# Kernel optimization log

Measured on AMD Instinct MI355X. Metric: run time of the kernel, lower is better.

Reference implementation:

```python
import jax, jax.numpy as jnp
import numpy as np
import math

B, T, EMB, HD = 4, 2048, 2048, 128
HALF = HD // 2


def setup_inputs() -> dict:
    key = jax.random.key(0)
    ks = jax.random.split(key, 4)
    x = jax.random.normal(ks[0], (B, T, EMB), dtype=jnp.float32)
    s = 1.0 / math.sqrt(EMB)
    Wq = jax.random.normal(ks[1], (EMB, HD), dtype=jnp.float32) * s
    Wk = jax.random.normal(ks[2], (EMB, HD), dtype=jnp.float32) * s
    Wv = jax.random.normal(ks[3], (EMB, HD), dtype=jnp.float32) * s
    # Standard RoPE rotation table: theta_i = 10000^(-2i/HD), angle = pos * theta
    inv_freq = 1.0 / (10000.0 ** (np.arange(0, HALF, dtype=np.float32) / HALF))
    angles = np.arange(T, dtype=np.float32)[:, None] * inv_freq[None, :]  # [T, HALF]
    rot_cos = jnp.asarray(np.cos(angles), dtype=jnp.float32)
    rot_sin = jnp.asarray(np.sin(angles), dtype=jnp.float32)
    # Additive causal mask: 0 on/below diagonal, -1e9 above
    NEG = -1e9
    mask = jnp.where(jnp.tril(jnp.ones((T, T), dtype=bool)), 0.0, NEG).astype(jnp.float32)
    return {"x": x, "Wq": Wq, "Wk": Wk, "Wv": Wv,
            "rot_cos": rot_cos, "rot_sin": rot_sin, "mask": mask}


def _apply_rope(q, rot_cos, rot_sin):
    # q: [B, T, HD]; view last dim as HALF complex pairs and rotate
    qp = q.reshape(q.shape[0], q.shape[1], HALF, 2)
    re, im = qp[..., 0], qp[..., 1]
    out_re = re * rot_cos - im * rot_sin  # broadcast [T,HALF] over batch
    out_im = re * rot_sin + im * rot_cos
    return jnp.stack([out_re, out_im], axis=-1).reshape(q.shape)


def reference(x, Wq, Wk, Wv, rot_cos, rot_sin, mask):
    Q = x @ Wq  # [B, T, HD]
    K = x @ Wk
    V = x @ Wv
    Q = _apply_rope(Q, rot_cos, rot_sin)
    K = _apply_rope(K, rot_cos, rot_sin)
    scores = jnp.einsum('bqd,bkd->bqk', Q, K) / math.sqrt(HD)
    probs = jax.nn.softmax(scores + mask, axis=-1)  # dropout is identity in eval
    return jnp.einsum('bqk,bkd->bqd', probs, V)
```

## Files before the change

### kernel.cpp

```cpp
#include <hip/hip_runtime.h>
#include <cstddef>
#include <cstdint>

#define T_SEQ 2048
#define EMB_D 2048
#define HD_D  128

typedef __attribute__((ext_vector_type(8))) short short8;
typedef __attribute__((ext_vector_type(4))) float f32x4;
typedef __attribute__((ext_vector_type(4))) unsigned short ushort4v;
typedef __attribute__((ext_vector_type(8))) unsigned short ushort8v;

union frag_u { short8 s8; unsigned u[4]; };

static __device__ __forceinline__ unsigned short f2bf_rne(float f) {
    union { float f; unsigned u; } v; v.f = f;
    unsigned r = v.u + 0x7fffu + ((v.u >> 16) & 1u);
    return (unsigned short)(r >> 16);
}
static __device__ __forceinline__ unsigned short f2bf_fast(float f) {
    union { float f; unsigned u; } v; v.f = f;
    return (unsigned short)((v.u + 0x8000u) >> 16);
}
static __device__ __forceinline__ float bf2f(unsigned short h) {
    union { unsigned u; float f; } v; v.u = ((unsigned)h) << 16;
    return v.f;
}
static __device__ __forceinline__ unsigned pk2(float a, float b) {
    union { float f; unsigned u; } x, y; x.f = a; y.f = b;
    return __builtin_amdgcn_perm(y.u + 0x8000u, x.u + 0x8000u, 0x07060302);
}
static __device__ __forceinline__ void dma16(const void* g, void* l) {
    __builtin_amdgcn_global_load_lds(
        (const __attribute__((address_space(1))) unsigned int*)g,
        (__attribute__((address_space(3))) unsigned int*)l, 16, 0, 0);
}
#define EXP2F(x) __builtin_amdgcn_exp2f(x)

__global__ __launch_bounds__(256) void prep_weights(
    const float* __restrict__ Wq, const float* __restrict__ Wk,
    const float* __restrict__ Wv, unsigned short* __restrict__ Wt)
{
    __shared__ __attribute__((aligned(16))) unsigned short tw[64 * 132];
    const int w = blockIdx.y;
    const int k0 = blockIdx.x * 64;
    const float* W = (w == 0) ? Wq : (w == 1) ? Wk : Wv;
    const int tid = threadIdx.x;
#pragma unroll
    for (int p = 0; p < 8; p++) {
        const int f = p * 256 + tid;
        const int row = f >> 5, c4 = f & 31;
        const float4 v = *(const float4*)&W[(size_t)(k0 + row) * HD_D + c4 * 4];
        ushort4v h = { f2bf_rne(v.x), f2bf_rne(v.y), f2bf_rne(v.z), f2bf_rne(v.w) };
        *(ushort4v*)&tw[row * 132 + c4 * 4] = h;
    }
    __syncthreads();
    const int kk = (tid & 7) * 8;
#pragma unroll
    for (int p = 0; p < 4; p++) {
        const int n = p * 32 + (tid >> 3);
        ushort8v o;
#pragma unroll
        for (int jj = 0; jj < 8; jj++) o[jj] = tw[(kk + jj) * 132 + n];
        *(ushort8v*)&Wt[(size_t)w * (HD_D * EMB_D) + (size_t)n * EMB_D + k0 + kk] = o;
    }
}

__global__ __launch_bounds__(256, 2) void qkv_fused(
    const float* __restrict__ x, const unsigned short* __restrict__ Wt,
    const float* __restrict__ rcos, const float* __restrict__ rsin,
    unsigned short* __restrict__ Qb, unsigned short* __restrict__ Kb,
    unsigned short* __restrict__ Vt)
{
    __shared__ __attribute__((aligned(16))) float xs[3][64 * 64];
    __shared__ __attribute__((aligned(16))) unsigned short wsb[2][96 * 64];
    const int L = blockIdx.x;
    const int xcd = L & 7, s = L >> 3;
    const int ng = s & 3;
    const int m0 = (xcd * 16 + (s >> 2)) * 64;
    const int tid = threadIdx.x;
    const int lane = tid & 63, wave = tid >> 6;
    const int wm = wave >> 1, wn = wave & 1;
    const int l15 = lane & 15, lq = lane >> 4;

    const float* xSrc[4]; int xOff[4];
#pragma unroll
    for (int p = 0; p < 4; p++) {
        const int g = p * 256 + tid;
        const int row = g >> 4, c = g & 15;
        xSrc[p] = x + (size_t)(m0 + row) * EMB_D + (c ^ (row & 15)) * 4;
        xOff[p] = (p * 256 + wave * 64) * 4;
    }
    const unsigned short* wSrc[3]; int wOff[3];
#pragma unroll
    for (int p = 0; p < 3; p++) {
        const int g = p * 256 + tid;
        const int row = g >> 3, c = g & 7;
        wSrc[p] = Wt + (size_t)(ng * 96 + row) * EMB_D + (c ^ (row & 7)) * 8;
        wOff[p] = (p * 256 + wave * 64) * 8;
    }

    int offA[2][2][2];
#pragma unroll
    for (int i = 0; i < 2; i++)
#pragma unroll
        for (int ks = 0; ks < 2; ks++) {
            const int row = wm * 32 + i * 16 + l15;
            const int ga = ks * 8 + lq * 2;
            offA[i][ks][0] = row * 64 + ((ga)     ^ (row & 15)) * 4;
            offA[i][ks][1] = row * 64 + ((ga + 1) ^ (row & 15)) * 4;
        }
    int offB[3][2];
#pragma unroll
    for (int j = 0; j < 3; j++)
#pragma unroll
        for (int ks = 0; ks < 2; ks++) {
            const int row = wn * 48 + j * 16 + l15;
            const int gb = ks * 4 + lq;
            offB[j][ks] = row * 64 + (gb ^ (row & 7)) * 8;
        }

    f32x4 acc[2][3];
#pragma unroll
    for (int i = 0; i < 2; i++)
#pragma unroll
        for (int j = 0; j < 3; j++) acc[i][j] = (f32x4){0.f, 0.f, 0.f, 0.f};

#pragma unroll
    for (int p = 0; p < 4; p++) dma16(xSrc[p], &xs[0][xOff[p]]);
#pragma unroll
    for (int p = 0; p < 3; p++) dma16(wSrc[p], &wsb[0][wOff[p]]);
#pragma unroll
    for (int p = 0; p < 4; p++) dma16(xSrc[p] + 64, &xs[1][xOff[p]]);

#define QKV_COMPUTE(XB, WB)                                                    \
    do {                                                                       \
        frag_u A[2][2];                                                        \
        _Pragma("unroll")                                                      \
        for (int i = 0; i < 2; i++)                                            \
            _Pragma("unroll")                                                  \
            for (int ks = 0; ks < 2; ks++) {                                   \
                const f32x4 f0 = *(const f32x4*)&xs[XB][offA[i][ks][0]];       \
                const f32x4 f1 = *(const f32x4*)&xs[XB][offA[i][ks][1]];       \
                A[i][ks].u[0] = pk2(f0.x, f0.y);                               \
                A[i][ks].u[1] = pk2(f0.z, f0.w);                               \
                A[i][ks].u[2] = pk2(f1.x, f1.y);                               \
                A[i][ks].u[3] = pk2(f1.z, f1.w);                               \
            }                                                                  \
        _Pragma("unroll")                                                      \
        for (int ks = 0; ks < 2; ks++)                                         \
            _Pragma("unroll")                                                  \
            for (int j = 0; j < 3; j++) {                                      \
                const short8 B = *(const short8*)&wsb[WB][offB[j][ks]];        \
                _Pragma("unroll")                                              \
                for (int i = 0; i < 2; i++)                                    \
                    acc[i][j] = __builtin_amdgcn_mfma_f32_16x16x32_bf16(       \
                        A[i][ks].s8, B, acc[i][j], 0, 0, 0);                   \
            }                                                                  \
    } while (0)

    for (int k0 = 0; k0 < EMB_D - 64; k0 += 64) {
        const int it = k0 >> 6;
        asm volatile("s_waitcnt vmcnt(4)\n\ts_barrier" ::: "memory");
#pragma unroll
        for (int p = 0; p < 3; p++)
            dma16(wSrc[p] + k0 + 64, &wsb[(it + 1) & 1][wOff[p]]);
        if (k0 + 128 < EMB_D) {
#pragma unroll
            for (int p = 0; p < 4; p++)
                dma16(xSrc[p] + k0 + 128, &xs[(it + 2) % 3][xOff[p]]);
        }
        QKV_COMPUTE(it % 3, it & 1);
    }
    asm volatile("s_waitcnt vmcnt(0)\n\ts_barrier" ::: "memory");
    QKV_COMPUTE(31 % 3, 31 & 1);
#undef QKV_COMPUTE

    const float qscale = 0.08838834764831845f * 1.4426950408889634f;
#pragma unroll
    for (int i = 0; i < 2; i++) {
#pragma unroll
        for (int r = 0; r < 4; r++) {
            const int row = m0 + wm * 32 + i * 16 + lq * 4 + r;
            const int t = row & (T_SEQ - 1);
            const int bb = row >> 11;
#pragma unroll
            for (int j = 0; j < 3; j++) {
                const int col = ng * 96 + wn * 48 + j * 16 + l15;
                const int mat = col >> 7, mcol = col & 127;
                const float v = acc[i][j][r];
                if (mat == 2) {
                    Vt[((size_t)bb * HD_D + mcol) * T_SEQ + t] = f2bf_rne(v);
                } else {
                    const int ip = mcol >> 1;
                    const float c = rcos[t * 64 + ip];
                    const float s2 = rsin[t * 64 + ip];
                    const float pv = __shfl_xor(v, 1);
                    float rv = (mcol & 1) ? (pv * s2 + v * c) : (v * c - pv * s2);
                    if (mat == 0) {
                        rv *= qscale;
                        Qb[(size_t)row * HD_D + mcol] = f2bf_rne(rv);
                    } else {
                        Kb[(size_t)row * HD_D + mcol] = f2bf_rne(rv);
                    }
                }
            }
        }
    }
}

__global__ __launch_bounds__(256, 2) void attn(
    const unsigned short* __restrict__ Qb, const unsigned short* __restrict__ Kb,
    const unsigned short* __restrict__ Vt, float* __restrict__ O0,
    unsigned short* __restrict__ O1, float* __restrict__ Lp)
{
    __shared__ __attribute__((aligned(16))) unsigned short O_s[4][16 * 128];
    __shared__ __attribute__((aligned(16))) unsigned short P_s[4][2][16 * 40];
    __shared__ float l_s[4][16];

    const int tid = threadIdx.x;
    const int lane = tid & 63, wave = tid >> 6;
    const int l15 = lane & 15, lq = lane >> 4;
    const int kf = lq * 8;

    const int L = blockIdx.x;
    const int g = L & 1;
    const int b = (L >> 1) & 3;
    const int q0 = (127 - (L >> 3)) * 16;
    const int kend = q0 + 16;
    const float M2 = 16.0f;

    const unsigned short* Qp = Qb + (size_t)(b * T_SEQ + q0) * HD_D;
    short8 aQ[4];
#pragma unroll
    for (int d = 0; d < 4; d++)
        aQ[d] = *(const short8*)&Qp[l15 * HD_D + d * 32 + kf];

    f32x4 acc[8];
#pragma unroll
    for (int d = 0; d < 8; d++) acc[d] = (f32x4){0.f, 0.f, 0.f, 0.f};
    float l_r[4] = {0.f, 0.f, 0.f, 0.f};

    const unsigned short* Kbase = Kb + (size_t)b * T_SEQ * HD_D;
    const unsigned short* Vbase = Vt + (size_t)b * HD_D * T_SEQ;
    unsigned short* PwA = &P_s[wave][0][0];
    unsigned short* PwB = &P_s[wave][1][0];

    for (int c = 2 * wave + g; c * 32 < kend; c += 16) {
        const int kA = c * 32;
        const int kB = (c + 8) * 32;
        const bool hB = kB < kend;

        const unsigned short* KpA = Kbase + (size_t)kA * HD_D;
        const unsigned short* KpB = Kbase + (size_t)kB * HD_D;
        short8 KA[8], KB_[8];
#pragma unroll
        for (int d = 0; d < 4; d++)
#pragma unroll
            for (int n = 0; n < 2; n++)
                KA[d * 2 + n] = *(const short8*)&KpA[(size_t)(n * 16 + l15) * HD_D + d * 32 + kf];
        if (hB) {
#pragma unroll
            for (int d = 0; d < 4; d++)
#pragma unroll
                for (int n = 0; n < 2; n++)
                    KB_[d * 2 + n] = *(const short8*)&KpB[(size_t)(n * 16 + l15) * HD_D + d * 32 + kf];
        }

        f32x4 sA0 = (f32x4){0.f, 0.f, 0.f, 0.f}, sA1 = sA0, sB0 = sA0, sB1 = sA0;
#pragma unroll
        for (int d = 0; d < 4; d++) {
            sA0 = __builtin_amdgcn_mfma_f32_16x16x32_bf16(aQ[d], KA[d * 2 + 0], sA0, 0, 0, 0);
            sA1 = __builtin_amdgcn_mfma_f32_16x16x32_bf16(aQ[d], KA[d * 2 + 1], sA1, 0, 0, 0);
        }
        if (hB) {
#pragma unroll
            for (int d = 0; d < 4; d++) {
                sB0 = __builtin_amdgcn_mfma_f32_16x16x32_bf16(aQ[d], KB_[d * 2 + 0], sB0, 0, 0, 0);
                sB1 = __builtin_amdgcn_mfma_f32_16x16x32_bf16(aQ[d], KB_[d * 2 + 1], sB1, 0, 0, 0);
            }
        }

        short8 VA[8];
#pragma unroll
        for (int d = 0; d < 8; d++)
            VA[d] = *(const short8*)&Vbase[(size_t)(d * 16 + l15) * T_SEQ + kA + kf];

#pragma unroll
        for (int r = 0; r < 4; r++) {
            const int q = q0 + lq * 4 + r;
            const float p0 = ((kA + l15)      <= q) ? EXP2F(sA0[r] - M2) : 0.f;
            const float p1 = ((kA + 16 + l15) <= q) ? EXP2F(sA1[r] - M2) : 0.f;
            l_r[r] += p0 + p1;
            const int prow = (lq * 4 + r) * 40;
            PwA[prow + l15]      = f2bf_fast(p0);
            PwA[prow + 16 + l15] = f2bf_fast(p1);
        }
        const short8 pA = *(const short8*)&PwA[l15 * 40 + kf];
#pragma unroll
        for (int d = 0; d < 8; d++)
            acc[d] = __builtin_amdgcn_mfma_f32_16x16x32_bf16(pA, VA[d], acc[d], 0, 0, 0);

        if (hB) {
            short8 VB[8];
#pragma unroll
            for (int d = 0; d < 8; d++)
                VB[d] = *(const short8*)&Vbase[(size_t)(d * 16 + l15) * T_SEQ + kB + kf];
#pragma unroll
            for (int r = 0; r < 4; r++) {
                const int q = q0 + lq * 4 + r;
                const float p0 = ((kB + l15)      <= q) ? EXP2F(sB0[r] - M2) : 0.f;
                const float p1 = ((kB + 16 + l15) <= q) ? EXP2F(sB1[r] - M2) : 0.f;
                l_r[r] += p0 + p1;
                const int prow = (lq * 4 + r) * 40;
                PwB[prow + l15]      = f2bf_fast(p0);
                PwB[prow + 16 + l15] = f2bf_fast(p1);
            }
            const short8 pB = *(const short8*)&PwB[l15 * 40 + kf];
#pragma unroll
            for (int d = 0; d < 8; d++)
                acc[d] = __builtin_amdgcn_mfma_f32_16x16x32_bf16(pB, VB[d], acc[d], 0, 0, 0);
        }
    }

#pragma unroll
    for (int r = 0; r < 4; r++) {
        float lr = l_r[r];
        lr += __shfl_xor(lr, 1);
        lr += __shfl_xor(lr, 2);
        lr += __shfl_xor(lr, 4);
        lr += __shfl_xor(lr, 8);
        if (l15 == 0) l_s[wave][lq * 4 + r] = lr;
#pragma unroll
        for (int d = 0; d < 8; d++)
            O_s[wave][(lq * 4 + r) * 128 + d * 16 + l15] = f2bf_fast(acc[d][r]);
    }
    __syncthreads();

    const int row = tid >> 4;
    const int dc = (tid & 15) * 8;
    const float lt = l_s[0][row] + l_s[1][row] + l_s[2][row] + l_s[3][row];
    float o[8];
#pragma unroll
    for (int k = 0; k < 8; k++) o[k] = 0.f;
#pragma unroll
    for (int w2 = 0; w2 < 4; w2++) {
        const ushort8v pv = *(const ushort8v*)&O_s[w2][row * 128 + dc];
#pragma unroll
        for (int k = 0; k < 8; k++) o[k] += bf2f(pv[k]);
    }
    const size_t grow = (size_t)(b * T_SEQ + q0 + row);
    if (g == 0) {
        float* op = O0 + grow * HD_D + dc;
#pragma unroll
        for (int k = 0; k < 8; k++) op[k] = o[k];
    } else {
        ushort8v h;
#pragma unroll
        for (int k = 0; k < 8; k++) h[k] = f2bf_fast(o[k]);
        *(ushort8v*)&O1[grow * HD_D + dc] = h;
    }
    if ((tid & 15) == 0) Lp[g * 8192 + grow] = lt;
}

__global__ __launch_bounds__(256) void attn_merge(
    float* __restrict__ out, const unsigned short* __restrict__ O1,
    const float* __restrict__ Lp)
{
    const int idx = blockIdx.x * 256 + threadIdx.x;
    const int row = idx >> 5;
    f32x4 a = ((f32x4*)out)[idx];
    const ushort4v h = ((const ushort4v*)O1)[idx];
    f32x4 bv = { bf2f(h.x), bf2f(h.y), bf2f(h.z), bf2f(h.w) };
    const float inv = 1.0f / (Lp[row] + Lp[8192 + row]);
    ((f32x4*)out)[idx] = (a + bv) * inv;
}

extern "C" void kernel_launch(void* const* d_in, const int* in_sizes, int n_in,
                              void* d_out, int out_size, void* d_ws, size_t ws_size,
                              hipStream_t stream)
{
    (void)in_sizes; (void)n_in; (void)out_size; (void)ws_size;
    const float* x  = (const float*)d_in[0];
    const float* Wq = (const float*)d_in[1];
    const float* Wk = (const float*)d_in[2];
    const float* Wv = (const float*)d_in[3];
    const float* rc = (const float*)d_in[4];
    const float* rs = (const float*)d_in[5];
    float* out = (float*)d_out;

    char* ws = (char*)d_ws;
    unsigned short* Wt = (unsigned short*)(ws);
    unsigned short* Qb = (unsigned short*)(ws + 1572864);
    unsigned short* Kb = (unsigned short*)(ws + 3670016);
    unsigned short* Vt = (unsigned short*)(ws + 5767168);
    unsigned short* O1 = (unsigned short*)(ws + 7864320);
    float*          Lp = (float*)(ws + 9961472);

    prep_weights<<<dim3(32, 3), 256, 0, stream>>>(Wq, Wk, Wv, Wt);
    qkv_fused   <<<dim3(512),   256, 0, stream>>>(x, Wt, rc, rs, Qb, Kb, Vt);
    attn        <<<dim3(1024),  256, 0, stream>>>(Qb, Kb, Vt, out, O1, Lp);
    attn_merge  <<<dim3(1024),  256, 0, stream>>>(out, O1, Lp);
}
```

Baseline: 188.4 us.

## Stage QKV GEMM tiles through registers with bf16 conversion before LDS

The QKV projection GEMM no longer uses direct global-to-LDS DMA of fp32 x tiles with per-iteration conversion. It now loads x and weight tiles into registers two steps ahead, converts x to bf16 once, and writes swizzled bf16 tiles into double-buffered LDS. Each wave then reads ready-made bf16 fragments and raises its scheduling priority around the MFMA block. This halves the LDS footprint for x, removes repeated packing in the inner loop, and may allow higher occupancy. In exchange it uses more registers for the in-flight data and adds explicit LDS store and wait steps.

```diff
diff --git a/kernel.cpp b/kernel.cpp
--- a/kernel.cpp
+++ b/kernel.cpp
@@ -10,8 +10,7 @@
 typedef __attribute__((ext_vector_type(4))) float f32x4;
 typedef __attribute__((ext_vector_type(4))) unsigned short ushort4v;
 typedef __attribute__((ext_vector_type(8))) unsigned short ushort8v;
-
-union frag_u { short8 s8; unsigned u[4]; };
+typedef __attribute__((ext_vector_type(2))) unsigned int uint2v;
 
 static __device__ __forceinline__ unsigned short f2bf_rne(float f) {
     union { float f; unsigned u; } v; v.f = f;
@@ -29,11 +28,6 @@
 static __device__ __forceinline__ unsigned pk2(float a, float b) {
     union { float f; unsigned u; } x, y; x.f = a; y.f = b;
     return __builtin_amdgcn_perm(y.u + 0x8000u, x.u + 0x8000u, 0x07060302);
-}
-static __device__ __forceinline__ void dma16(const void* g, void* l) {
-    __builtin_amdgcn_global_load_lds(
-        (const __attribute__((address_space(1))) unsigned int*)g,
-        (__attribute__((address_space(3))) unsigned int*)l, 16, 0, 0);
 }
 #define EXP2F(x) __builtin_amdgcn_exp2f(x)
 
@@ -72,8 +66,8 @@
     unsigned short* __restrict__ Qb, unsigned short* __restrict__ Kb,
     unsigned short* __restrict__ Vt)
 {
-    __shared__ __attribute__((aligned(16))) float xs[3][64 * 64];
-    __shared__ __attribute__((aligned(16))) unsigned short wsb[2][96 * 64];
+    __shared__ __attribute__((aligned(16))) unsigned short xsm[2][64 * 64];
+    __shared__ __attribute__((aligned(16))) unsigned short wsm[2][96 * 64];
     const int L = blockIdx.x;
     const int xcd = L & 7, s = L >> 3;
     const int ng = s & 3;
@@ -83,41 +77,28 @@
     const int wm = wave >> 1, wn = wave & 1;
     const int l15 = lane & 15, lq = lane >> 4;
 
-    const float* xSrc[4]; int xOff[4];
-#pragma unroll
-    for (int p = 0; p < 4; p++) {
-        const int g = p * 256 + tid;
-        const int row = g >> 4, c = g & 15;
-        xSrc[p] = x + (size_t)(m0 + row) * EMB_D + (c ^ (row & 15)) * 4;
-        xOff[p] = (p * 256 + wave * 64) * 4;
-    }
-    const unsigned short* wSrc[3]; int wOff[3];
-#pragma unroll
-    for (int p = 0; p < 3; p++) {
-        const int g = p * 256 + tid;
-        const int row = g >> 3, c = g & 7;
-        wSrc[p] = Wt + (size_t)(ng * 96 + row) * EMB_D + (c ^ (row & 7)) * 8;
-        wOff[p] = (p * 256 + wave * 64) * 8;
-    }
-
-    int offA[2][2][2];
+    const int xrow = tid >> 4, xc = tid & 15;
+    const float* xsrc = x + (size_t)(m0 + xrow) * EMB_D + xc * 4;
+    const int wrow = tid >> 3, wc = tid & 7;
+    const unsigned short* wsrc = Wt + (size_t)(ng * 96 + wrow) * EMB_D + wc * 8;
+
+    const int xw  = xrow * 128 + (((xc >> 1) ^ (xrow & 7)) << 4) + (xc & 1) * 8;
+    const int wwo = wrow * 128 + ((wc ^ (wrow & 7)) << 4);
+
+    int ra[2][2], rb[3][2];
 #pragma unroll
     for (int i = 0; i < 2; i++)
 #pragma unroll
         for (int ks = 0; ks < 2; ks++) {
             const int row = wm * 32 + i * 16 + l15;
-            const int ga = ks * 8 + lq * 2;
-            offA[i][ks][0] = row * 64 + ((ga)     ^ (row & 15)) * 4;
-            offA[i][ks][1] = row * 64 + ((ga + 1) ^ (row & 15)) * 4;
-        }
-    int offB[3][2];
-#pragma unroll
-    for (int j = 0; j < 3; j++)
+            ra[i][ks] = row * 128 + (((ks * 4 + lq) ^ (row & 7)) << 4);
+        }
+#pragma unroll
+    for (int jj = 0; jj < 3; jj++)
 #pragma unroll
         for (int ks = 0; ks < 2; ks++) {
-            const int row = wn * 48 + j * 16 + l15;
-            const int gb = ks * 4 + lq;
-            offB[j][ks] = row * 64 + (gb ^ (row & 7)) * 8;
+            const int row = wn * 48 + jj * 16 + l15;
+            rb[jj][ks] = row * 128 + (((ks * 4 + lq) ^ (row & 7)) << 4);
         }
 
     f32x4 acc[2][3];
@@ -126,55 +107,80 @@
 #pragma unroll
         for (int j = 0; j < 3; j++) acc[i][j] = (f32x4){0.f, 0.f, 0.f, 0.f};
 
-#pragma unroll
-    for (int p = 0; p < 4; p++) dma16(xSrc[p], &xs[0][xOff[p]]);
-#pragma unroll
-    for (int p = 0; p < 3; p++) dma16(wSrc[p], &wsb[0][wOff[p]]);
-#pragma unroll
-    for (int p = 0; p < 4; p++) dma16(xSrc[p] + 64, &xs[1][xOff[p]]);
-
-#define QKV_COMPUTE(XB, WB)                                                    \
-    do {                                                                       \
-        frag_u A[2][2];                                                        \
-        _Pragma("unroll")                                                      \
-        for (int i = 0; i < 2; i++)                                            \
-            _Pragma("unroll")                                                  \
-            for (int ks = 0; ks < 2; ks++) {                                   \
-                const f32x4 f0 = *(const f32x4*)&xs[XB][offA[i][ks][0]];       \
-                const f32x4 f1 = *(const f32x4*)&xs[XB][offA[i][ks][1]];       \
-                A[i][ks].u[0] = pk2(f0.x, f0.y);                               \
-                A[i][ks].u[1] = pk2(f0.z, f0.w);                               \
-                A[i][ks].u[2] = pk2(f1.x, f1.y);                               \
-                A[i][ks].u[3] = pk2(f1.z, f1.w);                               \
-            }                                                                  \
-        _Pragma("unroll")                                                      \
-        for (int ks = 0; ks < 2; ks++)                                         \
-            _Pragma("unroll")                                                  \
-            for (int j = 0; j < 3; j++) {                                      \
-                const short8 B = *(const short8*)&wsb[WB][offB[j][ks]];        \
-                _Pragma("unroll")                                              \
-                for (int i = 0; i < 2; i++)                                    \
-                    acc[i][j] = __builtin_amdgcn_mfma_f32_16x16x32_bf16(       \
-                        A[i][ks].s8, B, acc[i][j], 0, 0, 0);                   \
-            }                                                                  \
+    float4 xr[2][4];
+    short8 wr[2][3];
+
+#define LOADN(SET, K)                                                             \
+    do {                                                                          \
+        _Pragma("unroll")                                                         \
+        for (int p = 0; p < 4; p++)                                               \
+            xr[SET][p] = *(const float4*)(xsrc + (size_t)p * (16 * EMB_D) + (K)); \
+        _Pragma("unroll")                                                         \
+        for (int p = 0; p < 3; p++)                                               \
+            wr[SET][p] = *(const short8*)(wsrc + (size_t)p * (32 * EMB_D) + (K)); \
     } while (0)
 
-    for (int k0 = 0; k0 < EMB_D - 64; k0 += 64) {
-        const int it = k0 >> 6;
-        asm volatile("s_waitcnt vmcnt(4)\n\ts_barrier" ::: "memory");
-#pragma unroll
-        for (int p = 0; p < 3; p++)
-            dma16(wSrc[p] + k0 + 64, &wsb[(it + 1) & 1][wOff[p]]);
-        if (k0 + 128 < EMB_D) {
-#pragma unroll
-            for (int p = 0; p < 4; p++)
-                dma16(xSrc[p] + k0 + 128, &xs[(it + 2) % 3][xOff[p]]);
-        }
-        QKV_COMPUTE(it % 3, it & 1);
-    }
-    asm volatile("s_waitcnt vmcnt(0)\n\ts_barrier" ::: "memory");
-    QKV_COMPUTE(31 % 3, 31 & 1);
-#undef QKV_COMPUTE
+#define STAGE(SET, BUF)                                                           \
+    do {                                                                          \
+        char* xb = (char*)&xsm[BUF][0];                                           \
+        char* wb = (char*)&wsm[BUF][0];                                           \
+        _Pragma("unroll")                                                         \
+        for (int p = 0; p < 4; p++) {                                             \
+            uint2v u;                                                             \
+            u.x = pk2(xr[SET][p].x, xr[SET][p].y);                                \
+            u.y = pk2(xr[SET][p].z, xr[SET][p].w);                                \
+            *(uint2v*)(xb + xw + p * 2048) = u;                                   \
+        }                                                                         \
+        _Pragma("unroll")                                                         \
+        for (int p = 0; p < 3; p++)                                               \
+            *(short8*)(wb + wwo + p * 4096) = wr[SET][p];                         \
+    } while (0)
+
+#define COMPUTE(BUF)                                                              \
+    do {                                                                          \
+        const char* xb = (const char*)&xsm[BUF][0];                               \
+        const char* wb = (const char*)&wsm[BUF][0];                               \
+        short8 Af[2][2];                                                          \
+        _Pragma("unroll")                                                         \
+        for (int i = 0; i < 2; i++)                                               \
+            _Pragma("unroll")                                                     \
+            for (int ks = 0; ks < 2; ks++)                                        \
+                Af[i][ks] = *(const short8*)(xb + ra[i][ks]);                     \
+        __builtin_amdgcn_s_setprio(1);                                            \
+        _Pragma("unroll")                                                         \
+        for (int ks = 0; ks < 2; ks++)                                            \
+            _Pragma("unroll")                                                     \
+            for (int jj = 0; jj < 3; jj++) {                                      \
+                const short8 Bf = *(const short8*)(wb + rb[jj][ks]);              \
+                _Pragma("unroll")                                                 \
+                for (int i = 0; i < 2; i++)                                       \
+                    acc[i][jj] = __builtin_amdgcn_mfma_f32_16x16x32_bf16(         \
+                        Af[i][ks], Bf, acc[i][jj], 0, 0, 0);                      \
+            }                                                                     \
+        __builtin_amdgcn_s_setprio(0);                                            \
+    } while (0)
+
+#define BARX() asm volatile("s_waitcnt lgkmcnt(0)\n\ts_barrier" ::: "memory")
+
+    LOADN(0, 0);
+    LOADN(1, 64);
+    STAGE(0, 0);
+    LOADN(0, 128);
+
+#pragma clang loop unroll(disable)
+    for (int j = 0; j < 28; j += 2) {
+        BARX(); STAGE(1, 1); LOADN(1, (j + 3) * 64); COMPUTE(0);
+        BARX(); STAGE(0, 0); LOADN(0, (j + 4) * 64); COMPUTE(1);
+    }
+    BARX(); STAGE(1, 1); LOADN(1, 31 * 64); COMPUTE(0);
+    BARX(); STAGE(0, 0);                    COMPUTE(1);
+    BARX(); STAGE(1, 1);                    COMPUTE(0);
+    BARX();                                 COMPUTE(1);
+
+#undef LOADN
+#undef STAGE
+#undef COMPUTE
+#undef BARX
 
     const float qscale = 0.08838834764831845f * 1.4426950408889634f;
 #pragma unroll
```

New measurement: 179.9 us. 4.5% less time.
